# Optimization experiments

Measured on AMD Instinct MI355X. Metric: run time of the kernel, lower is better.

## Reference

```python
import jax, jax.numpy as jnp
import numpy as np
import math

OUT_H, OUT_W = 608 // 4, 1088 // 4   # 152, 272
HW = OUT_H * OUT_W                   # 41344
MAX_OBJS = 256
N_ANN = 64
NID = 537
EMB_DIM = 256
EMB_SCALE = math.sqrt(2.0) * math.log(NID - 1.0)
B = 8


def gaussian_radius(height, width, min_overlap=0.7):
    # standard CenterNet radius; height/width are jnp.ceil'd box sizes
    b1 = height + width
    c1 = width * height * (1.0 - min_overlap) / (1.0 + min_overlap)
    r1 = (b1 + jnp.sqrt(jnp.maximum(b1 * b1 - 4.0 * c1, 0.0))) / 2.0
    b2 = 2.0 * (height + width)
    c2 = (1.0 - min_overlap) * width * height
    r2 = (b2 + jnp.sqrt(jnp.maximum(b2 * b2 - 16.0 * c2, 0.0))) / 2.0
    b3 = -2.0 * min_overlap * (height + width)
    c3 = (min_overlap - 1.0) * width * height
    r3 = (b3 + jnp.sqrt(jnp.maximum(b3 * b3 - 16.0 * min_overlap * c3, 0.0))) / 2.0
    return jnp.minimum(jnp.minimum(r1, r2), r3)


def build_targets(ann1, ann2):
    # ann cols: [cx, cy, w, h, cls, pid, vis, extra]; boxes normalized to [0,1]
    cx_raw = ann1[:, 0] * OUT_W
    cy_raw = ann1[:, 1] * OUT_H
    w = ann1[:, 2] * OUT_W
    h = ann1[:, 3] * OUT_H
    # amodal box from UNclipped center (torch deepcopies before clipping)
    x1 = cx_raw - 0.5 * w; y1 = cy_raw - 0.5 * h
    x2 = x1 + w;           y2 = y1 + h
    cx = jnp.clip(cx_raw, 0.0, OUT_W - 1.0)
    cy = jnp.clip(cy_raw, 0.0, OUT_H - 1.0)
    ctx = cx.astype(jnp.int32)
    cty = cy.astype(jnp.int32)
    radius = jnp.maximum(jnp.floor(gaussian_radius(jnp.ceil(h), jnp.ceil(w))), 0.0)

    # batched gaussian splat, max-reduced over objects (draw_umich_gaussian)
    sigma = (2.0 * radius + 1.0) / 6.0
    dx = jnp.arange(OUT_W, dtype=jnp.float32)[None, :] - ctx[:, None].astype(jnp.float32)  # [N,W]
    dy = jnp.arange(OUT_H, dtype=jnp.float32)[None, :] - cty[:, None].astype(jnp.float32)  # [N,H]
    g = jnp.exp(-(dy[:, :, None] ** 2 + dx[:, None, :] ** 2) / (2.0 * sigma[:, None, None] ** 2))  # [N,H,W]
    win = (jnp.abs(dy)[:, :, None] <= radius[:, None, None]) & (jnp.abs(dx)[:, None, :] <= radius[:, None, None])
    hm = jnp.max(jnp.where(win, g, 0.0), axis=0)  # [H,W]

    # first match of each object's pid in the next frame (torch breaks at first hit)
    pid1 = ann1[:, 5]
    match = pid1[:, None] == ann2[None, :, 5]
    has = match.any(axis=1)
    t1 = ann2[jnp.argmax(match, axis=1)]
    cx2 = t1[:, 0] * OUT_W; cy2 = t1[:, 1] * OUT_H
    w2 = t1[:, 2] * OUT_W;  h2 = t1[:, 3] * OUT_H
    x1t = cx2 - 0.5 * w2; y1t = cy2 - 0.5 * h2
    x2t = x1t + w2;       y2t = y1t + h2

    valid = has & (h > 0) & (w > 0) & (h2 > 0) & (w2 > 0)
    vm = valid.astype(jnp.float32)
    cxf = ctx.astype(jnp.float32); cyf = cty.astype(jnp.float32)
    wh = jnp.stack([cxf - x1, x2 - cxf, cyf - y1, y2 - cyf,
                    cxf - x1t, x2t - cxf, cyf - y1t, y2t - cyf], axis=-1) * vm[:, None]
    ind = jnp.where(valid, cty * OUT_W + ctx, 0)
    v = ann1[:, 6] * vm
    ids = jnp.where(valid, pid1.astype(jnp.int32), 0)

    pad = MAX_OBJS - N_ANN
    return (hm,
            jnp.pad(ind, (0, pad)),
            jnp.pad(vm, (0, pad)),
            jnp.pad(wh, ((0, pad), (0, 0))),
            jnp.pad(v, (0, pad)),
            jnp.pad(ids, (0, pad)))


def focal_loss(pred, gt):
    # CenterNet focal loss; pred already sigmoid+clamped
    pos = (gt == 1.0).astype(pred.dtype)
    pos_loss = (jnp.log(pred) * (1.0 - pred) ** 2 * pos).sum()
    neg_loss = (jnp.log(1.0 - pred) * pred ** 2 * (1.0 - gt) ** 4 * (1.0 - pos)).sum()
    num_pos = pos.sum()
    return jnp.where(num_pos > 0, -(pos_loss + neg_loss) / jnp.maximum(num_pos, 1.0), -neg_loss)


def reg_loss(feat, mask, ind, target):
    # feat [C,HW]; gather per-object channels, masked smooth-L1 sum / num_valid
    pred = feat[:, ind].T                       # [max_objs, C]
    m = mask[:, None]
    d = jnp.abs(pred * m - target * m)
    sl1 = jnp.where(d < 1.0, 0.5 * d * d, d - 0.5)
    return sl1.sum() / (mask.sum() + 1e-4)


def id_loss(identi, ind, mask, v, ids, W_id, b_id):
    feat = identi[:, ind].T                     # [max_objs, 256]
    feat = EMB_SCALE * feat / jnp.maximum(jnp.linalg.norm(feat, axis=-1, keepdims=True), 1e-12)
    logits = feat @ W_id.T + b_id               # [max_objs, 537]
    logp = jax.nn.log_softmax(logits, axis=-1)
    nll = -v * jnp.take_along_axis(logp, ids[:, None], axis=1)[:, 0]
    return (nll * mask).sum() / jnp.maximum(mask.sum(), 1.0)


def reference(classifications, regressions, viss, identis, annotations1, annotations2, W_id, b_id, s_det, s_id):
    cls = jnp.clip(jax.nn.sigmoid(classifications), 1e-4, 1.0 - 1e-4)   # [B,1,HW]
    vis = jnp.clip(jax.nn.sigmoid(viss), 1e-4, 1.0 - 1e-4)              # [B,1,HW]
    hm, ind, mask, wh, v, ids = jax.vmap(build_targets)(annotations1, annotations2)
    cls_l = jax.vmap(lambda p, g: focal_loss(p.reshape(OUT_H, OUT_W), g))(cls, hm)
    reg_l = jax.vmap(reg_loss)(regressions, mask, ind, wh)
    vis_l = jax.vmap(lambda f, m, i, t: reg_loss(f, m, i, t[:, None]))(vis, mask, ind, v)
    id_l = jax.vmap(lambda f, i, m, vv, ii: id_loss(f, i, m, vv, ii, W_id, b_id))(identis, ind, mask, v, ids)
    return (cls_l.mean(keepdims=True), reg_l.mean(keepdims=True), vis_l.mean(keepdims=True),
            id_l.mean(keepdims=True), s_det, s_id)


def setup_inputs() -> dict:
    key = jax.random.key(0)
    ks = jax.random.split(key, 8)
    classifications = jax.random.normal(ks[0], (B, 1, HW), dtype=jnp.float32)
    regressions = jax.random.normal(ks[1], (B, 8, HW), dtype=jnp.float32)
    viss = jax.random.normal(ks[2], (B, 1, HW), dtype=jnp.float32)
    identis = jax.random.normal(ks[3], (B, EMB_DIM, HW), dtype=jnp.float32)

    def make_frame_pair(k):
        k1, k2, k3, k4, k5, k6, k7 = jax.random.split(k, 7)
        cx = jax.random.uniform(k1, (N_ANN,), minval=0.05, maxval=0.95)
        cy = jax.random.uniform(k2, (N_ANN,), minval=0.05, maxval=0.95)
        w = jax.random.uniform(k3, (N_ANN,), minval=0.02, maxval=0.25)
        h = jax.random.uniform(k4, (N_ANN,), minval=0.05, maxval=0.4)
        pid = jax.random.permutation(k5, NID)[:N_ANN].astype(jnp.float32)  # unique track ids
        vis = jax.random.uniform(k6, (N_ANN,))
        extra = jax.random.uniform(k7, (N_ANN,))
        cls = jnp.zeros((N_ANN,), dtype=jnp.float32)
        a1 = jnp.stack([cx, cy, w, h, cls, pid, vis, extra], axis=-1)
        kp, kj = jax.random.split(jax.random.fold_in(k, 99))
        a2 = a1[jax.random.permutation(kp, N_ANN)]
        a2 = a2.at[:, 0:2].add(0.01 * jax.random.normal(kj, (N_ANN, 2)))
        a2 = a2.at[:, 0:2].set(jnp.clip(a2[:, 0:2], 0.05, 0.95))
        return a1, a2

    pairs = [make_frame_pair(jax.random.fold_in(ks[4], b)) for b in range(B)]
    annotations1 = jnp.stack([p[0] for p in pairs])
    annotations2 = jnp.stack([p[1] for p in pairs])
    W_id = 0.02 * jax.random.normal(ks[5], (NID, EMB_DIM), dtype=jnp.float32)
    b_id = jnp.zeros((NID,), dtype=jnp.float32)
    s_det = jnp.array([-1.85], dtype=jnp.float32)
    s_id = jnp.array([-1.05], dtype=jnp.float32)
    return {"classifications": classifications, "regressions": regressions, "viss": viss,
            "identis": identis, "annotations1": annotations1, "annotations2": annotations2,
            "W_id": W_id, "b_id": b_id, "s_det": s_det, "s_id": s_id}
```

## Files before the change

kernel.cpp:

```cpp
#include <hip/hip_runtime.h>
#include <math.h>

#define OUT_H 152
#define OUT_W 272
#define HW 41344
#define NOBJ 64
#define NB 8
#define NID 537
#define EMB 256

#define NFBLK 162
#define NFOCAL (NFBLK * NB)
#define NIDBLK (NB * NOBJ)

#define OF_FP    0
#define OF_IDNLL (NFOCAL * 3)

__device__ inline float waveRedSum(float v) {
  for (int off = 32; off; off >>= 1) v += __shfl_down(v, off, 64);
  return v;
}
__device__ inline float waveRedMax(float v) {
  for (int off = 32; off; off >>= 1) v = fmaxf(v, __shfl_down(v, off, 64));
  return v;
}

struct PrepOut {
  float cxf, cyf, radius, inv2s2, vm, v;
  float wh[8];
  int ind, id;
};

__device__ __forceinline__ PrepOut prep_obj(const float* __restrict__ ann1,
                                            const float* __restrict__ ann2,
                                            int b, int i) {
  const float* a1 = ann1 + (b * NOBJ + i) * 8;
  const float* A2 = ann2 + b * NOBJ * 8;

  float cx_raw = a1[0] * (float)OUT_W;
  float cy_raw = a1[1] * (float)OUT_H;
  float w = a1[2] * (float)OUT_W;
  float h = a1[3] * (float)OUT_H;
  float x1 = cx_raw - 0.5f * w, y1 = cy_raw - 0.5f * h;
  float x2 = x1 + w, y2 = y1 + h;
  float cx = fminf(fmaxf(cx_raw, 0.f), (float)(OUT_W - 1));
  float cy = fminf(fmaxf(cy_raw, 0.f), (float)(OUT_H - 1));
  int ctx = (int)cx, cty = (int)cy;

  float hc = ceilf(h), wc = ceilf(w);
  float b1 = hc + wc;
  float c1 = wc * hc * 0.3f / 1.7f;
  float r1 = (b1 + sqrtf(fmaxf(b1 * b1 - 4.f * c1, 0.f))) * 0.5f;
  float b2 = 2.f * (hc + wc);
  float c2 = 0.3f * wc * hc;
  float r2 = (b2 + sqrtf(fmaxf(b2 * b2 - 16.f * c2, 0.f))) * 0.5f;
  float b3 = -1.4f * (hc + wc);
  float c3 = -0.3f * wc * hc;
  float r3 = (b3 + sqrtf(fmaxf(b3 * b3 - 11.2f * c3, 0.f))) * 0.5f;
  float radius = fmaxf(floorf(fminf(fminf(r1, r2), r3)), 0.f);
  float sigma = (2.f * radius + 1.f) / 6.f;

  PrepOut P;
  P.cxf = (float)ctx;
  P.cyf = (float)cty;
  P.radius = radius;
  P.inv2s2 = 1.f / (2.f * sigma * sigma);

  float pid = a1[5];
  int jm = -1;
  for (int j = 0; j < NOBJ; ++j) {
    if (A2[j * 8 + 5] == pid) { jm = j; break; }
  }
  bool has = (jm >= 0);
  const float* t1 = A2 + (has ? jm : 0) * 8;
  float cx2 = t1[0] * (float)OUT_W, cy2 = t1[1] * (float)OUT_H;
  float w2 = t1[2] * (float)OUT_W, h2 = t1[3] * (float)OUT_H;
  float x1t = cx2 - 0.5f * w2, y1t = cy2 - 0.5f * h2;
  float x2t = x1t + w2, y2t = y1t + h2;

  bool valid = has && (h > 0.f) && (w > 0.f) && (h2 > 0.f) && (w2 > 0.f);
  float vm = valid ? 1.f : 0.f;
  P.vm = vm;
  P.v = a1[6] * vm;
  P.wh[0] = (P.cxf - x1) * vm;  P.wh[1] = (x2 - P.cxf) * vm;
  P.wh[2] = (P.cyf - y1) * vm;  P.wh[3] = (y2 - P.cyf) * vm;
  P.wh[4] = (P.cxf - x1t) * vm; P.wh[5] = (x2t - P.cxf) * vm;
  P.wh[6] = (P.cyf - y1t) * vm; P.wh[7] = (y2t - P.cyf) * vm;
  P.ind = valid ? (cty * OUT_W + ctx) : 0;
  P.id = valid ? (int)pid : 0;
  return P;
}

__global__ void __launch_bounds__(256)
main_kernel(const float* __restrict__ cls,
            const float* __restrict__ identis,
            const float* __restrict__ W_id,
            const float* __restrict__ b_id,
            const float* __restrict__ ann1,
            const float* __restrict__ ann2,
            float* __restrict__ F) {
  if (blockIdx.x < NFOCAL) {
    int blk = blockIdx.x;
    int b = blk / NFBLK;
    int bx = blk - b * NFBLK;
    int p0 = bx * 256;
    int p = p0 + threadIdx.x;

    __shared__ unsigned s_pk[64];
    __shared__ float s_inv[64];
    __shared__ unsigned long long s_mask;
    if (threadIdx.x < 64) {
      PrepOut P = prep_obj(ann1, ann2, b, threadIdx.x);
      int ctx = (int)P.cxf, cty = (int)P.cyf, r = (int)P.radius;
      s_pk[threadIdx.x]  = (unsigned)ctx | ((unsigned)cty << 9) | ((unsigned)r << 17);
      s_inv[threadIdx.x] = P.inv2s2;
      int y0 = p0 / OUT_W;
      int y1 = (p0 + 255) / OUT_W;
      bool two_rows = (y1 > y0);
      int x0 = two_rows ? 0 : (p0 - y0 * OUT_W);
      int x1 = two_rows ? (OUT_W - 1) : (p0 + 255 - y0 * OUT_W);
      bool act = (cty + r >= y0) && (cty - r <= y1) &&
                 (ctx + r >= x0) && (ctx - r <= x1);
      unsigned long long m = __ballot(act);
      if (threadIdx.x == 0) s_mask = m;
    }
    __syncthreads();

    float pos_l = 0.f, neg_l = 0.f, npos = 0.f;
    if (p < HW) {
      float xf = (float)(p % OUT_W);
      float yf = (float)(p / OUT_W);
      float gt = 0.f;
      unsigned long long m = s_mask;
      while (m) {
        int o = __ffsll((unsigned long long)m) - 1;
        m &= m - 1;
        unsigned pk = s_pk[o];
        float inv = s_inv[o];
        float cxv = (float)(pk & 511u);
        float cyv = (float)((pk >> 9) & 255u);
        float rv  = (float)(pk >> 17);
        float dy = yf - cyv;
        float dx = xf - cxv;
        if (fabsf(dy) <= rv && fabsf(dx) <= rv) {
          gt = fmaxf(gt, __expf(-(dy * dy + dx * dx) * inv));
        }
      }
      float x = cls[b * HW + p];
      float pr = 1.f / (1.f + __expf(-x));
      pr = fminf(fmaxf(pr, 1e-4f), 0.9999f);
      if (gt == 1.f) {
        float om = 1.f - pr;
        pos_l = __logf(pr) * om * om;
        npos = 1.f;
      } else {
        float omg = 1.f - gt;
        float w4 = omg * omg;
        w4 *= w4;
        neg_l = __logf(1.f - pr) * pr * pr * w4;
      }
    }

    __shared__ float red[3][4];
    int wid = threadIdx.x >> 6, lane = threadIdx.x & 63;
    float a = waveRedSum(pos_l);
    float c = waveRedSum(neg_l);
    float n = waveRedSum(npos);
    if (lane == 0) { red[0][wid] = a; red[1][wid] = c; red[2][wid] = n; }
    __syncthreads();
    if (threadIdx.x == 0) {
      float pa = 0.f, pc = 0.f, pn = 0.f;
      for (int k = 0; k < 4; ++k) { pa += red[0][k]; pc += red[1][k]; pn += red[2][k]; }
      F[OF_FP + blk * 3 + 0] = pa;
      F[OF_FP + blk * 3 + 1] = pc;
      F[OF_FP + blk * 3 + 2] = pn;
    }
  } else {
    int o = blockIdx.x - NFOCAL;
    int b = o >> 6, i = o & 63;
    PrepOut P = prep_obj(ann1, ann2, b, i);
    if (P.vm == 0.f) {
      if (threadIdx.x == 0) F[OF_IDNLL + o] = 0.f;
      return;
    }
    int t = threadIdx.x;
    __shared__ float shf[EMB];
    __shared__ float slog[544];
    __shared__ float red4[4];
    int wid = t >> 6, lane = t & 63;

    float f = identis[(size_t)b * EMB * HW + (size_t)t * HW + P.ind];
    float n2 = waveRedSum(f * f);
    if (lane == 0) red4[wid] = n2;
    __syncthreads();
    float norm2 = red4[0] + red4[1] + red4[2] + red4[3];
    const float EMB_SCALE = 1.41421356237309515f * logf(536.0f);
    float scale = EMB_SCALE / fmaxf(sqrtf(norm2), 1e-12f);
    shf[t] = f * scale;
    __syncthreads();

    for (int c = t; c < NID; c += 256) {
      float acc = b_id[c];
      const float* wr = W_id + (size_t)c * EMB;
      #pragma unroll 8
      for (int k = 0; k < EMB; k += 4) {
        float4 wv = *(const float4*)(wr + k);
        float4 sv = *(const float4*)(&shf[k]);
        acc += wv.x * sv.x + wv.y * sv.y + wv.z * sv.z + wv.w * sv.w;
      }
      slog[c] = acc;
    }
    __syncthreads();

    float mx = -1e30f;
    for (int c = t; c < NID; c += 256) mx = fmaxf(mx, slog[c]);
    mx = waveRedMax(mx);
    __syncthreads();
    if (lane == 0) red4[wid] = mx;
    __syncthreads();
    mx = fmaxf(fmaxf(red4[0], red4[1]), fmaxf(red4[2], red4[3]));

    float se = 0.f;
    for (int c = t; c < NID; c += 256) se += __expf(slog[c] - mx);
    se = waveRedSum(se);
    __syncthreads();
    if (lane == 0) red4[wid] = se;
    __syncthreads();

    if (t == 0) {
      float sesum = red4[0] + red4[1] + red4[2] + red4[3];
      float lse = mx + __logf(sesum);
      F[OF_IDNLL + o] = -P.v * (slog[P.id] - lse);
    }
  }
}

__global__ void __launch_bounds__(512)
final_kernel(const float* __restrict__ reg,
             const float* __restrict__ viss,
             const float* __restrict__ ann1,
             const float* __restrict__ ann2,
             const float* __restrict__ F,
             const float* __restrict__ s_det,
             const float* __restrict__ s_id,
             float* __restrict__ out) {
  int t = threadIdx.x;
  int b = t >> 6;
  int lane = t & 63;

  PrepOut P = prep_obj(ann1, ann2, b, lane);
  float msum = waveRedSum(P.vm);

  float rsum = 0.f, vsum = 0.f;
  if (P.vm > 0.f) {
    for (int c = 0; c < 8; ++c) {
      float pred = reg[(b * 8 + c) * HW + P.ind];
      float d = fabsf(pred - P.wh[c]);
      rsum += (d < 1.f) ? 0.5f * d * d : d - 0.5f;
    }
    float s = 1.f / (1.f + __expf(-viss[b * HW + P.ind]));
    s = fminf(fmaxf(s, 1e-4f), 0.9999f);
    float d = fabsf(s - P.v);
    vsum += (d < 1.f) ? 0.5f * d * d : d - 0.5f;
  }
  rsum = waveRedSum(rsum);
  vsum = waveRedSum(vsum);

  float pa = 0.f, pc = 0.f, pn = 0.f;
  for (int e = lane; e < NFBLK; e += 64) {
    const float* fp = F + OF_FP + (b * NFBLK + e) * 3;
    pa += fp[0]; pc += fp[1]; pn += fp[2];
  }
  pa = waveRedSum(pa);
  pc = waveRedSum(pc);
  pn = waveRedSum(pn);

  float idv = waveRedSum(F[OF_IDNLL + b * 64 + lane]);

  __shared__ float L[8][4];
  if (lane == 0) {
    L[b][0] = (pn > 0.f) ? (-(pa + pc) / fmaxf(pn, 1.f)) : (-pc);
    L[b][1] = rsum / (msum + 0.0001f);
    L[b][2] = vsum / (msum + 0.0001f);
    L[b][3] = idv / fmaxf(msum, 1.f);
  }
  __syncthreads();
  if (t == 0) {
    float cl = 0.f, rl = 0.f, vl = 0.f, il = 0.f;
    for (int k = 0; k < 8; ++k) {
      cl += L[k][0]; rl += L[k][1]; vl += L[k][2]; il += L[k][3];
    }
    out[0] = cl / 8.f;
    out[1] = rl / 8.f;
    out[2] = vl / 8.f;
    out[3] = il / 8.f;
    out[4] = s_det[0];
    out[5] = s_id[0];
  }
}

extern "C" void kernel_launch(void* const* d_in, const int* in_sizes, int n_in,
                              void* d_out, int out_size, void* d_ws, size_t ws_size,
                              hipStream_t stream) {
  const float* cls     = (const float*)d_in[0];
  const float* reg     = (const float*)d_in[1];
  const float* viss    = (const float*)d_in[2];
  const float* identis = (const float*)d_in[3];
  const float* ann1    = (const float*)d_in[4];
  const float* ann2    = (const float*)d_in[5];
  const float* W_id    = (const float*)d_in[6];
  const float* b_id    = (const float*)d_in[7];
  const float* s_det   = (const float*)d_in[8];
  const float* s_id    = (const float*)d_in[9];
  float* F = (float*)d_ws;

  main_kernel<<<NFOCAL + NIDBLK, 256, 0, stream>>>(cls, identis, W_id, b_id,
                                                   ann1, ann2, F);
  final_kernel<<<1, 512, 0, stream>>>(reg, viss, ann1, ann2, F,
                                      s_det, s_id, (float*)d_out);
}
```

Baseline: 60.91 us.

## Batch four objects per ID block to reuse W_id loads across embeddings

```diff
diff --git a/kernel.cpp b/kernel.cpp
--- a/kernel.cpp
+++ b/kernel.cpp
@@ -11,17 +11,13 @@
 
 #define NFBLK 162
 #define NFOCAL (NFBLK * NB)
-#define NIDBLK (NB * NOBJ)
+#define NIDG   128
 
 #define OF_FP    0
 #define OF_IDNLL (NFOCAL * 3)
 
 __device__ inline float waveRedSum(float v) {
   for (int off = 32; off; off >>= 1) v += __shfl_down(v, off, 64);
-  return v;
-}
-__device__ inline float waveRedMax(float v) {
-  for (int off = 32; off; off >>= 1) v = fmaxf(v, __shfl_down(v, off, 64));
   return v;
 }
 
@@ -176,61 +172,128 @@
       F[OF_FP + blk * 3 + 2] = pn;
     }
   } else {
-    int o = blockIdx.x - NFOCAL;
-    int b = o >> 6, i = o & 63;
-    PrepOut P = prep_obj(ann1, ann2, b, i);
-    if (P.vm == 0.f) {
-      if (threadIdx.x == 0) F[OF_IDNLL + o] = 0.f;
-      return;
-    }
+    int g = blockIdx.x - NFOCAL;
+    int i = g >> 1;
+    int bh = g & 1;
     int t = threadIdx.x;
-    __shared__ float shf[EMB];
-    __shared__ float slog[544];
-    __shared__ float red4[4];
     int wid = t >> 6, lane = t & 63;
 
-    float f = identis[(size_t)b * EMB * HW + (size_t)t * HW + P.ind];
-    float n2 = waveRedSum(f * f);
-    if (lane == 0) red4[wid] = n2;
-    __syncthreads();
-    float norm2 = red4[0] + red4[1] + red4[2] + red4[3];
+    __shared__ int   s_ind[4], s_idv[4];
+    __shared__ float s_v[4];
+    __shared__ float sE[EMB][4];
+    __shared__ float slog[NID][4];
+    __shared__ float redn[4][4], redm[4][4], reds[4][4];
+
+    {
+      int b = bh * 4 + wid;
+      const float* a1 = ann1 + (b * NOBJ + i) * 8;
+      float w = a1[2] * (float)OUT_W;
+      float h = a1[3] * (float)OUT_H;
+      float cx = fminf(fmaxf(a1[0] * (float)OUT_W, 0.f), (float)(OUT_W - 1));
+      float cy = fminf(fmaxf(a1[1] * (float)OUT_H, 0.f), (float)(OUT_H - 1));
+      int ctx = (int)cx, cty = (int)cy;
+      float pid = a1[5];
+      const float* A2 = ann2 + b * NOBJ * 8;
+      bool mt = (A2[lane * 8 + 5] == pid);
+      unsigned long long bal = __ballot(mt);
+      bool has = (bal != 0ull);
+      int jm = has ? (__ffsll((unsigned long long)bal) - 1) : 0;
+      float w2 = A2[jm * 8 + 2] * (float)OUT_W;
+      float h2 = A2[jm * 8 + 3] * (float)OUT_H;
+      bool valid = has && (h > 0.f) && (w > 0.f) && (h2 > 0.f) && (w2 > 0.f);
+      if (lane == 0) {
+        s_ind[wid] = valid ? (cty * OUT_W + ctx) : 0;
+        s_idv[wid] = valid ? (int)pid : 0;
+        s_v[wid]   = valid ? a1[6] : 0.f;
+      }
+    }
+    __syncthreads();
+
+    float f0 = identis[(size_t)(bh * 4 + 0) * EMB * HW + (size_t)t * HW + s_ind[0]];
+    float f1 = identis[(size_t)(bh * 4 + 1) * EMB * HW + (size_t)t * HW + s_ind[1]];
+    float f2 = identis[(size_t)(bh * 4 + 2) * EMB * HW + (size_t)t * HW + s_ind[2]];
+    float f3 = identis[(size_t)(bh * 4 + 3) * EMB * HW + (size_t)t * HW + s_ind[3]];
+    {
+      float p0 = waveRedSum(f0 * f0);
+      float p1 = waveRedSum(f1 * f1);
+      float p2 = waveRedSum(f2 * f2);
+      float p3 = waveRedSum(f3 * f3);
+      if (lane == 0) {
+        redn[wid][0] = p0; redn[wid][1] = p1;
+        redn[wid][2] = p2; redn[wid][3] = p3;
+      }
+    }
+    __syncthreads();
     const float EMB_SCALE = 1.41421356237309515f * logf(536.0f);
-    float scale = EMB_SCALE / fmaxf(sqrtf(norm2), 1e-12f);
-    shf[t] = f * scale;
-    __syncthreads();
-
-    for (int c = t; c < NID; c += 256) {
-      float acc = b_id[c];
-      const float* wr = W_id + (size_t)c * EMB;
-      #pragma unroll 8
+    float sc0 = EMB_SCALE / fmaxf(sqrtf(redn[0][0]+redn[1][0]+redn[2][0]+redn[3][0]), 1e-12f);
+    float sc1 = EMB_SCALE / fmaxf(sqrtf(redn[0][1]+redn[1][1]+redn[2][1]+redn[3][1]), 1e-12f);
+    float sc2 = EMB_SCALE / fmaxf(sqrtf(redn[0][2]+redn[1][2]+redn[2][2]+redn[3][2]), 1e-12f);
+    float sc3 = EMB_SCALE / fmaxf(sqrtf(redn[0][3]+redn[1][3]+redn[2][3]+redn[3][3]), 1e-12f);
+    *(float4*)&sE[t][0] = make_float4(f0 * sc0, f1 * sc1, f2 * sc2, f3 * sc3);
+    __syncthreads();
+
+    {
+      const float* wr0 = W_id + (size_t)t * EMB;
+      const float* wr1 = W_id + (size_t)(t + 256) * EMB;
+      float A0=0.f,A1=0.f,A2v=0.f,A3=0.f, B0=0.f,B1=0.f,B2=0.f,B3=0.f;
       for (int k = 0; k < EMB; k += 4) {
-        float4 wv = *(const float4*)(wr + k);
-        float4 sv = *(const float4*)(&shf[k]);
-        acc += wv.x * sv.x + wv.y * sv.y + wv.z * sv.z + wv.w * sv.w;
-      }
-      slog[c] = acc;
-    }
-    __syncthreads();
-
+        float4 wa = *(const float4*)(wr0 + k);
+        float4 wb = *(const float4*)(wr1 + k);
+        float4 e0 = *(const float4*)&sE[k][0];
+        float4 e1 = *(const float4*)&sE[k + 1][0];
+        float4 e2 = *(const float4*)&sE[k + 2][0];
+        float4 e3 = *(const float4*)&sE[k + 3][0];
+        A0 += wa.x*e0.x + wa.y*e1.x + wa.z*e2.x + wa.w*e3.x;
+        A1 += wa.x*e0.y + wa.y*e1.y + wa.z*e2.y + wa.w*e3.y;
+        A2v+= wa.x*e0.z + wa.y*e1.z + wa.z*e2.z + wa.w*e3.z;
+        A3 += wa.x*e0.w + wa.y*e1.w + wa.z*e2.w + wa.w*e3.w;
+        B0 += wb.x*e0.x + wb.y*e1.x + wb.z*e2.x + wb.w*e3.x;
+        B1 += wb.x*e0.y + wb.y*e1.y + wb.z*e2.y + wb.w*e3.y;
+        B2 += wb.x*e0.z + wb.y*e1.z + wb.z*e2.z + wb.w*e3.z;
+        B3 += wb.x*e0.w + wb.y*e1.w + wb.z*e2.w + wb.w*e3.w;
+      }
+      float bb0 = b_id[t], bb1 = b_id[t + 256];
+      *(float4*)&slog[t][0]       = make_float4(A0+bb0, A1+bb0, A2v+bb0, A3+bb0);
+      *(float4*)&slog[t + 256][0] = make_float4(B0+bb1, B1+bb1, B2+bb1, B3+bb1);
+      if (t < NID - 512) {
+        int r2 = t + 512;
+        const float* wr2 = W_id + (size_t)r2 * EMB;
+        float C0=0.f,C1=0.f,C2=0.f,C3=0.f;
+        for (int k = 0; k < EMB; k += 4) {
+          float4 wc = *(const float4*)(wr2 + k);
+          float4 e0 = *(const float4*)&sE[k][0];
+          float4 e1 = *(const float4*)&sE[k + 1][0];
+          float4 e2 = *(const float4*)&sE[k + 2][0];
+          float4 e3 = *(const float4*)&sE[k + 3][0];
+          C0 += wc.x*e0.x + wc.y*e1.x + wc.z*e2.x + wc.w*e3.x;
+          C1 += wc.x*e0.y + wc.y*e1.y + wc.z*e2.y + wc.w*e3.y;
+          C2 += wc.x*e0.z + wc.y*e1.z + wc.z*e2.z + wc.w*e3.z;
+          C3 += wc.x*e0.w + wc.y*e1.w + wc.z*e2.w + wc.w*e3.w;
+        }
+        float bb2 = b_id[r2];
+        *(float4*)&slog[r2][0] = make_float4(C0+bb2, C1+bb2, C2+bb2, C3+bb2);
+      }
+    }
+    __syncthreads();
+
+    int j = t & 3;
     float mx = -1e30f;
-    for (int c = t; c < NID; c += 256) mx = fmaxf(mx, slog[c]);
-    mx = waveRedMax(mx);
-    __syncthreads();
-    if (lane == 0) red4[wid] = mx;
-    __syncthreads();
-    mx = fmaxf(fmaxf(red4[0], red4[1]), fmaxf(red4[2], red4[3]));
-
+    for (int r = (t >> 2); r < NID; r += 64) mx = fmaxf(mx, slog[r][j]);
+    for (int off = 32; off >= 4; off >>= 1) mx = fmaxf(mx, __shfl_xor(mx, off, 64));
+    if (lane < 4) redm[wid][lane] = mx;
+    __syncthreads();
+    float mxf = fmaxf(fmaxf(redm[0][j], redm[1][j]), fmaxf(redm[2][j], redm[3][j]));
     float se = 0.f;
-    for (int c = t; c < NID; c += 256) se += __expf(slog[c] - mx);
-    se = waveRedSum(se);
-    __syncthreads();
-    if (lane == 0) red4[wid] = se;
-    __syncthreads();
-
-    if (t == 0) {
-      float sesum = red4[0] + red4[1] + red4[2] + red4[3];
-      float lse = mx + __logf(sesum);
-      F[OF_IDNLL + o] = -P.v * (slog[P.id] - lse);
+    for (int r = (t >> 2); r < NID; r += 64) se += __expf(slog[r][j] - mxf);
+    for (int off = 32; off >= 4; off >>= 1) se += __shfl_xor(se, off, 64);
+    if (lane < 4) reds[wid][lane] = se;
+    __syncthreads();
+    if (t < 4) {
+      float set = reds[0][t] + reds[1][t] + reds[2][t] + reds[3][t];
+      float mxt = fmaxf(fmaxf(redm[0][t], redm[1][t]), fmaxf(redm[2][t], redm[3][t]));
+      float lse = mxt + __logf(set);
+      float nll = -s_v[t] * (slog[s_idv[t]][t] - lse);
+      F[OF_IDNLL + (bh * 4 + t) * 64 + i] = nll;
     }
   }
 }
@@ -314,8 +377,8 @@
   const float* s_id    = (const float*)d_in[9];
   float* F = (float*)d_ws;
 
-  main_kernel<<<NFOCAL + NIDBLK, 256, 0, stream>>>(cls, identis, W_id, b_id,
-                                                   ann1, ann2, F);
+  main_kernel<<<NFOCAL + NIDG, 256, 0, stream>>>(cls, identis, W_id, b_id,
+                                                 ann1, ann2, F);
   final_kernel<<<1, 512, 0, stream>>>(reg, viss, ann1, ann2, F,
                                       s_det, s_id, (float*)d_out);
 }
```

Result: no change. 61.27 us (+0.6%).
